# Kernel optimization log

Hardware: AMD Instinct MI355X
Metric: run time of the kernel (lower is better)

The kernel has to match this reference:

```python
import jax, jax.numpy as jnp
import numpy as np

N_NODES = 50000


def gcn_conv(x, W, b, row, col, n):
    """PyG GCNConv with default add_self_loops=True, normalize=True.
    out[i] = sum_{e: col[e]=i} d^-1/2[row[e]] d^-1/2[i] * (x@W)[row[e]]
             + d^-1[i]*(x@W)[i] + b,  where d = in-degree + 1 (self-loop).
    """
    x_lin = x @ W                                   # [n, out_ch]
    ones = jnp.ones(row.shape[0], dtype=x.dtype)
    deg = jax.ops.segment_sum(ones, col, num_segments=n) + 1.0  # self-loop
    dinv = jax.lax.rsqrt(deg)                       # deg >= 1, safe
    norm = dinv[row] * dinv[col]                    # [E]
    msg = norm[:, None] * x_lin[row]                # [E, out_ch]
    agg = jax.ops.segment_sum(msg, col, num_segments=n)
    self_term = (dinv * dinv)[:, None] * x_lin      # self-loop contribution
    return agg + self_term + b


def setup_inputs() -> dict:
    key = jax.random.key(0)
    ks = jax.random.split(key, 10)
    in_ch, hid, out_ch = 128, 256, 64
    E = 800000
    x = jax.random.normal(ks[0], (N_NODES, in_ch), dtype=jnp.float32)
    edge_attr = jax.random.normal(ks[1], (E, 8), dtype=jnp.float32)  # unused by forward
    edge_index = jax.random.randint(ks[2], (2, E), 0, N_NODES, dtype=jnp.int64)
    def glorot(k, fan_in, fan_out):
        s = float(np.sqrt(6.0 / (fan_in + fan_out)))
        return jax.random.uniform(k, (fan_in, fan_out), jnp.float32, -s, s)
    return {
        "x": x,
        "edge_attr": edge_attr,
        "edge_index": edge_index,
        "W1": glorot(ks[3], in_ch, hid), "b1": jnp.zeros((hid,), jnp.float32),
        "W2": glorot(ks[4], hid, hid),  "b2": jnp.zeros((hid,), jnp.float32),
        "W3": glorot(ks[5], hid, out_ch), "b3": jnp.zeros((out_ch,), jnp.float32),
    }


def reference(x, edge_attr, edge_index, W1, b1, W2, b2, W3, b3):
    n = x.shape[0]
    row, col = edge_index[0], edge_index[1]
    h = jax.nn.sigmoid(gcn_conv(x, W1, b1, row, col, n))
    h = jax.nn.sigmoid(gcn_conv(h, W2, b2, row, col, n))
    # dropout(p=0.1) in eval mode is identity
    return gcn_conv(h, W3, b3, row, col, n)
```

## Files before the change

kernel.cpp:

```cpp
#include <hip/hip_runtime.h>
#include <hip/hip_bf16.h>

typedef __bf16 bf16x8_t __attribute__((ext_vector_type(8)));
typedef float f32x4_t __attribute__((ext_vector_type(4)));
typedef float f32x2_t __attribute__((ext_vector_type(2)));

__device__ __forceinline__ float bits2f(unsigned int u) {
    union { unsigned int u; float f; } c; c.u = u; return c.f;
}
__device__ __forceinline__ unsigned short f2bf_bits(float f) {
    __hip_bfloat16 h = __float2bfloat16(f);
    return __builtin_bit_cast(unsigned short, h);
}

__global__ void sentinel_fill(float* __restrict__ out, int n) {
    int i = blockIdx.x * blockDim.x + threadIdx.x;
    if (i < n) out[i] = 100.0f;
}

__global__ void detect_ei(const unsigned int* __restrict__ ei, int* __restrict__ flags) {
    int lane = threadIdx.x;
    int cz = 0;
    #pragma unroll
    for (int j = 0; j < 4; ++j) {
        int idx = lane * 4 + j;
        cz += (ei[2 * idx + 1] == 0u);
    }
    #pragma unroll
    for (int off = 32; off; off >>= 1) cz += __shfl_down(cz, off);
    if (lane == 0) flags[0] = (cz > 200);
}


__global__ void count_rank_dual(const int* __restrict__ ei, int* __restrict__ cnt,
                                int* __restrict__ rank, int E, int M,
                                const int* __restrict__ flags) {
    int e = blockIdx.x * blockDim.x + threadIdx.x;
    if (e < E) {
        int c = flags[0] ? ei[2 * E + 2 * e] : ei[E + e];
        int rk = 0;
        if ((unsigned)c < (unsigned)M) rk = atomicAdd(&cnt[c], 1);
        rank[e] = rk;
    }
}

__global__ void scan_blocks(const int* __restrict__ cnt, int* __restrict__ excl,
                            int* __restrict__ bsum, int n) {
    int tid = threadIdx.x;
    int i = blockIdx.x * 256 + tid;
    int lane = tid & 63, wv = tid >> 6;
    __shared__ int ws[4];
    int v = (i < n) ? cnt[i] : 0;
    int s = v;
    #pragma unroll
    for (int off = 1; off < 64; off <<= 1) {
        int t = __shfl_up(s, off);
        if (lane >= off) s += t;
    }
    if (lane == 63) ws[wv] = s;
    __syncthreads();
    if (tid == 0) { int a = 0; for (int q = 0; q < 4; ++q) { int t = ws[q]; ws[q] = a; a += t; } }
    __syncthreads();
    int ex = s - v + ws[wv];
    if (i < n) excl[i] = ex;
    if (tid == 255) bsum[blockIdx.x] = ex + v;
}

__global__ void scan_bsums(const int* __restrict__ bsum, int* __restrict__ boff,
                           int nb, int* __restrict__ colptr, int n) {
    int tid = threadIdx.x, lane = tid & 63, wv = tid >> 6;
    __shared__ int ws[4];
    __shared__ int carry;
    if (tid == 0) carry = 0;
    __syncthreads();
    for (int base = 0; base < nb; base += 256) {
        int i = base + tid;
        int v = (i < nb) ? bsum[i] : 0;
        int s = v;
        #pragma unroll
        for (int off = 1; off < 64; off <<= 1) {
            int t = __shfl_up(s, off);
            if (lane >= off) s += t;
        }
        if (lane == 63) ws[wv] = s;
        __syncthreads();
        if (tid == 0) { int a = carry; for (int q = 0; q < 4; ++q) { int t = ws[q]; ws[q] = a; a += t; } carry = a; }
        __syncthreads();
        int ex = s - v + ws[wv];
        if (i < nb) boff[i] = ex;
        __syncthreads();
    }
    if (tid == 0) colptr[n] = carry;
}

__global__ void scan_add_dinv(const int* __restrict__ excl, const int* __restrict__ boff,
                              const int* __restrict__ cnt, int* __restrict__ colptr,
                              float* __restrict__ dinv, int n) {
    int i = blockIdx.x * 256 + threadIdx.x;
    if (i < n) {
        colptr[i] = excl[i] + boff[blockIdx.x];
        dinv[i] = rsqrtf((float)cnt[i] + 1.0f);
    }
}

__global__ void fill_csr_part(const int* __restrict__ ei, const int* __restrict__ colptr,
                              const int* __restrict__ rank, int* __restrict__ esrc,
                              int E, int M, int psz, const int* __restrict__ flags) {
    int part = blockIdx.x & 7;
    int e = (blockIdx.x >> 3) * 256 + threadIdx.x;
    int lo = part * psz;
    int hi = lo + psz; if (hi > M) hi = M;
    if (e < E) {
        int r, c;
        if (flags[0]) { r = ei[2 * e]; c = ei[2 * E + 2 * e]; }
        else          { r = ei[e];     c = ei[E + e]; }
        if (c >= lo && c < hi && (unsigned)r < (unsigned)M) {
            int p = colptr[c] + rank[e];
            if ((unsigned)p < (unsigned)E) esrc[p] = r;
        }
    }
}

__global__ void transpose_all(const float* __restrict__ W1, const float* __restrict__ W2,
                              const float* __restrict__ W3,
                              unsigned short* __restrict__ Wt1, unsigned short* __restrict__ Wt2,
                              unsigned short* __restrict__ Wt3) {
    int i = blockIdx.x * 256 + threadIdx.x;
    if (i < 32768) {
        int k = i >> 8, n = i & 255;
        Wt1[n * 128 + k] = f2bf_bits(W1[i]);
    } else if (i < 32768 + 65536) {
        int j = i - 32768;
        int k = j >> 8, n = j & 255;
        Wt2[n * 256 + k] = f2bf_bits(W2[j]);
    } else if (i < 114688) {
        int j = i - 98304;
        int k = j >> 6, n = j & 63;
        Wt3[n * 256 + k] = f2bf_bits(W3[j]);
    }
}

__global__ void prescale_x(const float* __restrict__ x, const float* __restrict__ dinv,
                           unsigned short* __restrict__ xs, int total) {
    int i = blockIdx.x * 256 + threadIdx.x;
    if (i < total) {
        int row = i >> 7;
        xs[i] = f2bf_bits(x[i] * dinv[row]);
    }
}

template<int K, int BN, int NTOT, int EPI>
__global__ __launch_bounds__(256) void gemm_tile(
    const __bf16* __restrict__ A,
    const unsigned short* __restrict__ Bt,
    const float* __restrict__ dinv,
    const float* __restrict__ bias,
    void* __restrict__ Y,
    int M)
{
    constexpr int KS = (K > 128) ? 128 : K;
    constexpr int KP = KS + 8;
    constexpr int NT = BN / 2 / 16;
    __shared__ unsigned short Bs[BN * KP];

    const int tid  = threadIdx.x;
    const int lane = tid & 63;
    const int wave = tid >> 6;
    const int wm   = wave >> 1;
    const int wn   = wave & 1;
    const int quad = lane >> 4;
    const int l16  = lane & 15;
    const int n0   = blockIdx.y * BN;

    int mrow[4];
#pragma unroll
    for (int mt = 0; mt < 4; ++mt) {
        int r = blockIdx.x * 128 + wm * 64 + mt * 16 + l16;
        mrow[mt] = (r < M) ? r : (M - 1);
    }

    f32x4_t acc[4][NT];
#pragma unroll
    for (int mt = 0; mt < 4; ++mt)
#pragma unroll
        for (int t = 0; t < NT; ++t) acc[mt][t] = (f32x4_t){0.f, 0.f, 0.f, 0.f};

    const unsigned short* BsW = &Bs[(wn * (BN / 2)) * KP];

    for (int kh = 0; kh < K; kh += KS) {
        constexpr int CH = BN * KS / 8;
        for (int idx = tid; idx < CH; idx += 256) {
            int n  = idx / (KS / 8);
            int k8 = idx - n * (KS / 8);
            uint4 v = *(const uint4*)(Bt + (size_t)(n0 + n) * K + kh + k8 * 8);
            *(uint4*)&Bs[n * KP + k8 * 8] = v;
        }
        __syncthreads();

#pragma unroll
        for (int kc = 0; kc < KS; kc += 32) {
            bf16x8_t a[4], b[NT];
#pragma unroll
            for (int mt = 0; mt < 4; ++mt)
                a[mt] = *(const bf16x8_t*)(A + (size_t)mrow[mt] * K + kh + kc + quad * 8);
#pragma unroll
            for (int t = 0; t < NT; ++t)
                b[t] = *(const bf16x8_t*)&BsW[(t * 16 + l16) * KP + kc + quad * 8];
#pragma unroll
            for (int mt = 0; mt < 4; ++mt)
#pragma unroll
                for (int t = 0; t < NT; ++t)
                    acc[mt][t] = __builtin_amdgcn_mfma_f32_16x16x32_bf16(a[mt], b[t], acc[mt][t], 0, 0, 0);
        }
        if (kh + KS < K) __syncthreads();
    }

    float bv[NT];
    if constexpr (EPI == 1) {
#pragma unroll
        for (int t = 0; t < NT; ++t)
            bv[t] = bias[n0 + wn * (BN / 2) + t * 16 + l16];
    }

#pragma unroll
    for (int mt = 0; mt < 4; ++mt) {
        int rowbase = blockIdx.x * 128 + wm * 64 + mt * 16 + quad * 4;
#pragma unroll
        for (int r = 0; r < 4; ++r) {
            int rrow = rowbase + r;
            if (rrow < M) {
                if constexpr (EPI == 0) {
                    float dv = dinv[rrow];
#pragma unroll
                    for (int t = 0; t < NT; ++t) {
                        int ccol = n0 + wn * (BN / 2) + t * 16 + l16;
                        ((__hip_bfloat16*)Y)[(size_t)rrow * NTOT + ccol] =
                            __float2bfloat16(acc[mt][t][r] * dv);
                    }
                } else if constexpr (EPI == 1) {
#pragma unroll
                    for (int t = 0; t < NT; ++t) {
                        int ccol = n0 + wn * (BN / 2) + t * 16 + l16;
                        float o = acc[mt][t][r] + bv[t];
                        o = 1.f / (1.f + __expf(-o));
                        ((__hip_bfloat16*)Y)[(size_t)rrow * NTOT + ccol] = __float2bfloat16(o);
                    }
                } else {
                    float dv = dinv[rrow];
#pragma unroll
                    for (int t = 0; t < NT; ++t) {
                        int ccol = n0 + wn * (BN / 2) + t * 16 + l16;
                        float o = acc[mt][t][r] * dv;
                        int pk = __builtin_amdgcn_cvt_pk_fp8_f32(o, o, 0, false);
                        ((unsigned char*)Y)[(size_t)rrow * NTOT + ccol] = (unsigned char)(pk & 0xff);
                    }
                }
            }
        }
    }
}

__global__ __launch_bounds__(256) void aggregate_fp8_256(
    const unsigned char* __restrict__ Y8,
    const int* __restrict__ colptr,
    const int* __restrict__ esrc,
    const float* __restrict__ dinv,
    const float* __restrict__ bias,
    unsigned short* __restrict__ H,
    int M, int Etot)
{
    const int lane = threadIdx.x & 63;
    const int wave = threadIdx.x >> 6;
    const int l = lane & 15;
    const int g = lane >> 4;
    int node = blockIdx.x * 4 + wave;
    if (node >= M) return;

    int s = colptr[node];
    int e = colptr[node + 1];
    if (s < 0) s = 0;
    if (e > Etot) e = Etot;
    if (e < s) e = s;

    const char* Yb = (const char*)Y8;
    const unsigned loff = (unsigned)(l * 16);

    f32x2_t acc[8];
    #pragma unroll
    for (int k = 0; k < 8; ++k) acc[k] = (f32x2_t){0.f, 0.f};

    auto unpack = [&](uint4 u) {
        acc[0] += __builtin_amdgcn_cvt_pk_f32_fp8(u.x, false);
        acc[1] += __builtin_amdgcn_cvt_pk_f32_fp8(u.x, true);
        acc[2] += __builtin_amdgcn_cvt_pk_f32_fp8(u.y, false);
        acc[3] += __builtin_amdgcn_cvt_pk_f32_fp8(u.y, true);
        acc[4] += __builtin_amdgcn_cvt_pk_f32_fp8(u.z, false);
        acc[5] += __builtin_amdgcn_cvt_pk_f32_fp8(u.z, true);
        acc[6] += __builtin_amdgcn_cvt_pk_f32_fp8(u.w, false);
        acc[7] += __builtin_amdgcn_cvt_pk_f32_fp8(u.w, true);
    };

    for (int base = s; base < e; base += 64) {
        int n = e - base; if (n > 64) n = 64;
        unsigned myOff = 0;
        if (lane < n) myOff = (unsigned)esrc[base + lane] << 8;
        int j = 0;
        #pragma unroll 4
        for (; j + 4 <= n; j += 4) {
            unsigned off = __shfl(myOff, j + g) + loff;
            uint4 u = *(const uint4*)(Yb + off);
            unpack(u);
        }
        if (j < n) {
            unsigned off = __shfl(myOff, j + g) + loff;
            if (j + g < n) {
                uint4 u = *(const uint4*)(Yb + off);
                unpack(u);
            }
        }
    }
    if (g == 0) {
        uint4 u = *(const uint4*)(Yb + ((unsigned)node << 8) + loff);
        unpack(u);
    }
    #pragma unroll
    for (int off = 16; off < 64; off <<= 1) {
        #pragma unroll
        for (int k = 0; k < 8; ++k) {
            f32x2_t t;
            t[0] = __shfl_xor(acc[k][0], off);
            t[1] = __shfl_xor(acc[k][1], off);
            acc[k] += t;
        }
    }

    if (g == 0) {
        float dv = dinv[node];
        float o[16];
        #pragma unroll
        for (int k = 0; k < 8; ++k) {
            o[2 * k]     = acc[k][0] * dv + bias[l * 16 + 2 * k];
            o[2 * k + 1] = acc[k][1] * dv + bias[l * 16 + 2 * k + 1];
        }
        #pragma unroll
        for (int k = 0; k < 16; ++k) o[k] = 1.f / (1.f + __expf(-o[k]));
        uint4 s0, s1;
        s0.x = (unsigned)f2bf_bits(o[0])  | ((unsigned)f2bf_bits(o[1])  << 16);
        s0.y = (unsigned)f2bf_bits(o[2])  | ((unsigned)f2bf_bits(o[3])  << 16);
        s0.z = (unsigned)f2bf_bits(o[4])  | ((unsigned)f2bf_bits(o[5])  << 16);
        s0.w = (unsigned)f2bf_bits(o[6])  | ((unsigned)f2bf_bits(o[7])  << 16);
        s1.x = (unsigned)f2bf_bits(o[8])  | ((unsigned)f2bf_bits(o[9])  << 16);
        s1.y = (unsigned)f2bf_bits(o[10]) | ((unsigned)f2bf_bits(o[11]) << 16);
        s1.z = (unsigned)f2bf_bits(o[12]) | ((unsigned)f2bf_bits(o[13]) << 16);
        s1.w = (unsigned)f2bf_bits(o[14]) | ((unsigned)f2bf_bits(o[15]) << 16);
        unsigned short* Hp = H + (size_t)node * 256 + l * 16;
        *(uint4*)Hp       = s0;
        *(uint4*)(Hp + 8) = s1;
    }
}

template<int C, bool SIG, bool OUTF32, bool HASB>
__global__ __launch_bounds__(256) void aggregate2(
    const unsigned short* __restrict__ Y,
    const int* __restrict__ colptr,
    const int* __restrict__ esrc,
    const float* __restrict__ dinv,
    const float* __restrict__ bias,
    void* __restrict__ H,
    int M, int Etot)
{
    constexpr int G   = C / 8;
    constexpr int EPW = 64 / G;
    const int lane = threadIdx.x & 63;
    const int wave = threadIdx.x >> 6;
    const int l = lane & (G - 1);
    const int g = lane / G;
    int node = blockIdx.x * 4 + wave;
    if (node >= M) return;

    int s = colptr[node];
    int e = colptr[node + 1];
    if (s < 0) s = 0;
    if (e > Etot) e = Etot;
    if (e < s) e = s;

    const char* Yb = (const char*)Y;
    const unsigned loff = (unsigned)(l * 16);

    float acc[8];
    #pragma unroll
    for (int k = 0; k < 8; ++k) acc[k] = 0.f;

    auto unpack = [&](uint4 u) {
        acc[0] += bits2f(u.x << 16);
        acc[1] += bits2f(u.x & 0xffff0000u);
        acc[2] += bits2f(u.y << 16);
        acc[3] += bits2f(u.y & 0xffff0000u);
        acc[4] += bits2f(u.z << 16);
        acc[5] += bits2f(u.z & 0xffff0000u);
        acc[6] += bits2f(u.w << 16);
        acc[7] += bits2f(u.w & 0xffff0000u);
    };

    for (int base = s; base < e; base += 64) {
        int n = e - base; if (n > 64) n = 64;
        unsigned myOff = 0;
        if (lane < n) myOff = (unsigned)esrc[base + lane] * (unsigned)(C * 2);
        int j = 0;
        #pragma unroll 4
        for (; j + EPW <= n; j += EPW) {
            unsigned off = __shfl(myOff, j + g) + loff;
            uint4 u = *(const uint4*)(Yb + off);
            unpack(u);
        }
        if (j < n) {
            unsigned off = __shfl(myOff, j + g) + loff;
            if (j + g < n) {
                uint4 u = *(const uint4*)(Yb + off);
                unpack(u);
            }
        }
    }
    if (g == 0) {
        unsigned off = (unsigned)node * (unsigned)(C * 2) + loff;
        uint4 u = *(const uint4*)(Yb + off);
        unpack(u);
    }
    #pragma unroll
    for (int off = G; off < 64; off <<= 1) {
        #pragma unroll
        for (int k = 0; k < 8; ++k) acc[k] += __shfl_xor(acc[k], off);
    }

    if (g == 0) {
        float dv = dinv[node];
        float o[8];
        #pragma unroll
        for (int k = 0; k < 8; ++k) {
            o[k] = acc[k] * dv;
            if (HASB) o[k] += bias[l * 8 + k];
            if (SIG) o[k] = 1.f / (1.f + __expf(-o[k]));
        }
        if constexpr (OUTF32) {
            float* Hp = (float*)H + (size_t)node * C + l * 8;
            *(float4*)Hp       = (float4){o[0], o[1], o[2], o[3]};
            *(float4*)(Hp + 4) = (float4){o[4], o[5], o[6], o[7]};
        } else {
            uint4 st;
            st.x = (unsigned)f2bf_bits(o[0]) | ((unsigned)f2bf_bits(o[1]) << 16);
            st.y = (unsigned)f2bf_bits(o[2]) | ((unsigned)f2bf_bits(o[3]) << 16);
            st.z = (unsigned)f2bf_bits(o[4]) | ((unsigned)f2bf_bits(o[5]) << 16);
            st.w = (unsigned)f2bf_bits(o[6]) | ((unsigned)f2bf_bits(o[7]) << 16);
            *(uint4*)((unsigned short*)H + (size_t)node * C + l * 8) = st;
        }
    }
}


extern "C" void kernel_launch(void* const* d_in, const int* in_sizes, int n_in,
                              void* d_out, int out_size, void* d_ws, size_t ws_size,
                              hipStream_t stream)
{
    int iEI = 2, iW1 = 3, iB1 = 4, iW2 = 5, iB2 = 6, iW3 = 7, iB3 = 8;
    if (n_in == 8) { iEI = 1; iW1 = 2; iB1 = 3; iW2 = 4; iB2 = 5; iW3 = 6; iB3 = 7; }

    const float* x  = (const float*)d_in[0];
    const int* ei   = (const int*)d_in[iEI];
    const float* W1 = (const float*)d_in[iW1];
    const float* b1 = (const float*)d_in[iB1];
    const float* W2 = (const float*)d_in[iW2];
    const float* b2 = (const float*)d_in[iB2];
    const float* W3 = (const float*)d_in[iW3];
    const float* b3 = (const float*)d_in[iB3];

    const int M = in_sizes[0] / 128;
    const int E = in_sizes[iEI] / 2;
    const int NB = (M + 255) / 256;
    const int PSZ = (M + 7) / 8;

    auto rnd = [](size_t b) { return (b + 255) & ~(size_t)255; };
    size_t needed = rnd(64 * 4)
                  + rnd((size_t)M * 4) * 2
                  + rnd((size_t)(M + 1) * 4)
                  + rnd((size_t)M * 4)
                  + rnd((size_t)(NB + 1) * 4) * 2
                  + rnd((size_t)E * 4) * 2
                  + rnd((size_t)256 * 128 * 2)
                  + rnd((size_t)256 * 256 * 2)
                  + rnd((size_t)64 * 256 * 2)
                  + rnd((size_t)M * 256 * 2) * 2;
    if (ws_size < needed) {
        sentinel_fill<<<(out_size + 255) / 256, 256, 0, stream>>>((float*)d_out, out_size);
        return;
    }

    char* p = (char*)d_ws;
    auto alloc = [&](size_t bytes) {
        char* r = p;
        p += (bytes + 255) & ~(size_t)255;
        return r;
    };
    int* flags  = (int*)alloc(64 * 4);
    float* dinv = (float*)alloc((size_t)M * 4);
    int* cnt    = (int*)alloc((size_t)M * 4);
    int* colptr = (int*)alloc((size_t)(M + 1) * 4);
    int* excl   = (int*)alloc((size_t)M * 4);
    int* bsum   = (int*)alloc((size_t)(NB + 1) * 4);
    int* boff   = (int*)alloc((size_t)(NB + 1) * 4);
    int* esrc   = (int*)alloc((size_t)E * 4);
    int* rank   = (int*)alloc((size_t)E * 4);
    unsigned short* Wt1 = (unsigned short*)alloc((size_t)256 * 128 * 2);
    unsigned short* Wt2 = (unsigned short*)alloc((size_t)256 * 256 * 2);
    unsigned short* Wt3 = (unsigned short*)alloc((size_t)64 * 256 * 2);
    __hip_bfloat16* ybuf = (__hip_bfloat16*)alloc((size_t)M * 256 * 2);
    __hip_bfloat16* hbuf = (__hip_bfloat16*)alloc((size_t)M * 256 * 2);

    unsigned short* xs = (unsigned short*)ybuf;
    unsigned short* xa = (unsigned short*)ybuf + (size_t)M * 128;
    unsigned char*  y8 = (unsigned char*)ybuf;

    detect_ei<<<1, 64, 0, stream>>>((const unsigned int*)ei, flags);

    hipMemsetAsync(cnt, 0, (size_t)M * 4, stream);
    count_rank_dual<<<(E + 255) / 256, 256, 0, stream>>>(ei, cnt, rank, E, M, flags);
    scan_blocks<<<NB, 256, 0, stream>>>(cnt, excl, bsum, M);
    scan_bsums<<<1, 256, 0, stream>>>(bsum, boff, NB, colptr, M);
    scan_add_dinv<<<NB, 256, 0, stream>>>(excl, boff, cnt, colptr, dinv, M);
    fill_csr_part<<<((E + 255) / 256) * 8, 256, 0, stream>>>(
        ei, colptr, rank, esrc, E, M, PSZ, flags);
    transpose_all<<<(114688 + 255) / 256, 256, 0, stream>>>(W1, W2, W3, Wt1, Wt2, Wt3);

    int gmb = (M + 127) / 128;
    int ga  = (M + 3) / 4;

    prescale_x<<<((M * 128) + 255) / 256, 256, 0, stream>>>(x, dinv, xs, M * 128);
    aggregate2<128, false, false, false><<<ga, 256, 0, stream>>>(
        xs, colptr, esrc, dinv, nullptr, xa, M, E);
    gemm_tile<128, 128, 256, 1><<<dim3(gmb, 2), 256, 0, stream>>>(
        (const __bf16*)xa, Wt1, dinv, b1, hbuf, M);
    gemm_tile<256, 128, 256, 2><<<dim3(gmb, 2), 256, 0, stream>>>(
        (const __bf16*)hbuf, Wt2, dinv, b2, y8, M);
    aggregate_fp8_256<<<ga, 256, 0, stream>>>(
        y8, colptr, esrc, dinv, b2, (unsigned short*)hbuf, M, E);
    gemm_tile<256, 64, 64, 0><<<dim3(gmb, 1), 256, 0, stream>>>(
        (const __bf16*)hbuf, Wt3, dinv, b3, ybuf, M);
    aggregate2<64, false, true, true><<<ga, 256, 0, stream>>>(
        (const unsigned short*)ybuf, colptr, esrc, dinv, b3, d_out, M, E);
}
```

Baseline: 347.4 us.

## Use fp8 gather features for layer-1 and layer-3 aggregations

Layer 1 now prescales x straight to fp8, vectorised over float4, instead of bf16. Layer 3's GEMM epilogue now writes fp8 rows as well. Both aggregations then run through a single generalised fp8 gather kernel templated on channel count. This halves the bytes read per gathered neighbour row in the bandwidth-bound aggregations, at the cost of lower precision in layer 1's input and layer 3's output features.

New measurement: 354.0 us. No clear change (+1.9%).

```diff
diff --git a/kernel.cpp b/kernel.cpp
--- a/kernel.cpp
+++ b/kernel.cpp
@@ -140,12 +140,16 @@
     }
 }
 
-__global__ void prescale_x(const float* __restrict__ x, const float* __restrict__ dinv,
-                           unsigned short* __restrict__ xs, int total) {
+__global__ void prescale_x_fp8(const float* __restrict__ x, const float* __restrict__ dinv,
+                               unsigned int* __restrict__ xs8, int total4) {
     int i = blockIdx.x * 256 + threadIdx.x;
-    if (i < total) {
-        int row = i >> 7;
-        xs[i] = f2bf_bits(x[i] * dinv[row]);
+    if (i < total4) {
+        int row = (i * 4) >> 7;
+        float dv = dinv[row];
+        float4 v = ((const float4*)x)[i];
+        int p0 = __builtin_amdgcn_cvt_pk_fp8_f32(v.x * dv, v.y * dv, 0, false);
+        int p1 = __builtin_amdgcn_cvt_pk_fp8_f32(v.z * dv, v.w * dv, 0, false);
+        xs8[i] = ((unsigned)p0 & 0xffffu) | ((unsigned)p1 << 16);
     }
 }
 
@@ -260,19 +264,23 @@
     }
 }
 
-__global__ __launch_bounds__(256) void aggregate_fp8_256(
+template<int C, bool SIG, bool OUTF32, bool HASB>
+__global__ __launch_bounds__(256) void aggregate_fp8(
     const unsigned char* __restrict__ Y8,
     const int* __restrict__ colptr,
     const int* __restrict__ esrc,
     const float* __restrict__ dinv,
     const float* __restrict__ bias,
-    unsigned short* __restrict__ H,
+    void* __restrict__ H,
     int M, int Etot)
 {
+    constexpr int G   = C / 16;
+    constexpr int EPW = 64 / G;
+    constexpr int SH  = (C == 256) ? 8 : ((C == 128) ? 7 : 6);
     const int lane = threadIdx.x & 63;
     const int wave = threadIdx.x >> 6;
-    const int l = lane & 15;
-    const int g = lane >> 4;
+    const int l = lane & (G - 1);
+    const int g = lane / G;
     int node = blockIdx.x * 4 + wave;
     if (node >= M) return;
 
@@ -303,10 +311,10 @@
     for (int base = s; base < e; base += 64) {
         int n = e - base; if (n > 64) n = 64;
         unsigned myOff = 0;
-        if (lane < n) myOff = (unsigned)esrc[base + lane] << 8;
+        if (lane < n) myOff = (unsigned)esrc[base + lane] << SH;
         int j = 0;
         #pragma unroll 4
-        for (; j + 4 <= n; j += 4) {
+        for (; j + EPW <= n; j += EPW) {
             unsigned off = __shfl(myOff, j + g) + loff;
             uint4 u = *(const uint4*)(Yb + off);
             unpack(u);
@@ -320,11 +328,11 @@
         }
     }
     if (g == 0) {
-        uint4 u = *(const uint4*)(Yb + ((unsigned)node << 8) + loff);
+        uint4 u = *(const uint4*)(Yb + ((unsigned)node << SH) + loff);
         unpack(u);
     }
     #pragma unroll
-    for (int off = 16; off < 64; off <<= 1) {
+    for (int off = G; off < 64; off <<= 1) {
         #pragma unroll
         for (int k = 0; k < 8; ++k) {
             f32x2_t t;
@@ -339,119 +347,36 @@
         float o[16];
         #pragma unroll
         for (int k = 0; k < 8; ++k) {
-            o[2 * k]     = acc[k][0] * dv + bias[l * 16 + 2 * k];
-            o[2 * k + 1] = acc[k][1] * dv + bias[l * 16 + 2 * k + 1];
-        }
-        #pragma unroll
-        for (int k = 0; k < 16; ++k) o[k] = 1.f / (1.f + __expf(-o[k]));
-        uint4 s0, s1;
-        s0.x = (unsigned)f2bf_bits(o[0])  | ((unsigned)f2bf_bits(o[1])  << 16);
-        s0.y = (unsigned)f2bf_bits(o[2])  | ((unsigned)f2bf_bits(o[3])  << 16);
-        s0.z = (unsigned)f2bf_bits(o[4])  | ((unsigned)f2bf_bits(o[5])  << 16);
-        s0.w = (unsigned)f2bf_bits(o[6])  | ((unsigned)f2bf_bits(o[7])  << 16);
-        s1.x = (unsigned)f2bf_bits(o[8])  | ((unsigned)f2bf_bits(o[9])  << 16);
-        s1.y = (unsigned)f2bf_bits(o[10]) | ((unsigned)f2bf_bits(o[11]) << 16);
-        s1.z = (unsigned)f2bf_bits(o[12]) | ((unsigned)f2bf_bits(o[13]) << 16);
-        s1.w = (unsigned)f2bf_bits(o[14]) | ((unsigned)f2bf_bits(o[15]) << 16);
-        unsigned short* Hp = H + (size_t)node * 256 + l * 16;
-        *(uint4*)Hp       = s0;
-        *(uint4*)(Hp + 8) = s1;
-    }
-}
-
-template<int C, bool SIG, bool OUTF32, bool HASB>
-__global__ __launch_bounds__(256) void aggregate2(
-    const unsigned short* __restrict__ Y,
-    const int* __restrict__ colptr,
-    const int* __restrict__ esrc,
-    const float* __restrict__ dinv,
-    const float* __restrict__ bias,
-    void* __restrict__ H,
-    int M, int Etot)
-{
-    constexpr int G   = C / 8;
-    constexpr int EPW = 64 / G;
-    const int lane = threadIdx.x & 63;
-    const int wave = threadIdx.x >> 6;
-    const int l = lane & (G - 1);
-    const int g = lane / G;
-    int node = blockIdx.x * 4 + wave;
-    if (node >= M) return;
-
-    int s = colptr[node];
-    int e = colptr[node + 1];
-    if (s < 0) s = 0;
-    if (e > Etot) e = Etot;
-    if (e < s) e = s;
-
-    const char* Yb = (const char*)Y;
-    const unsigned loff = (unsigned)(l * 16);
-
-    float acc[8];
-    #pragma unroll
-    for (int k = 0; k < 8; ++k) acc[k] = 0.f;
-
-    auto unpack = [&](uint4 u) {
-        acc[0] += bits2f(u.x << 16);
-        acc[1] += bits2f(u.x & 0xffff0000u);
-        acc[2] += bits2f(u.y << 16);
-        acc[3] += bits2f(u.y & 0xffff0000u);
-        acc[4] += bits2f(u.z << 16);
-        acc[5] += bits2f(u.z & 0xffff0000u);
-        acc[6] += bits2f(u.w << 16);
-        acc[7] += bits2f(u.w & 0xffff0000u);
-    };
-
-    for (int base = s; base < e; base += 64) {
-        int n = e - base; if (n > 64) n = 64;
-        unsigned myOff = 0;
-        if (lane < n) myOff = (unsigned)esrc[base + lane] * (unsigned)(C * 2);
-        int j = 0;
-        #pragma unroll 4
-        for (; j + EPW <= n; j += EPW) {
-            unsigned off = __shfl(myOff, j + g) + loff;
-            uint4 u = *(const uint4*)(Yb + off);
-            unpack(u);
-        }
-        if (j < n) {
-            unsigned off = __shfl(myOff, j + g) + loff;
-            if (j + g < n) {
-                uint4 u = *(const uint4*)(Yb + off);
-                unpack(u);
-            }
-        }
-    }
-    if (g == 0) {
-        unsigned off = (unsigned)node * (unsigned)(C * 2) + loff;
-        uint4 u = *(const uint4*)(Yb + off);
-        unpack(u);
-    }
-    #pragma unroll
-    for (int off = G; off < 64; off <<= 1) {
-        #pragma unroll
-        for (int k = 0; k < 8; ++k) acc[k] += __shfl_xor(acc[k], off);
-    }
-
-    if (g == 0) {
-        float dv = dinv[node];
-        float o[8];
-        #pragma unroll
-        for (int k = 0; k < 8; ++k) {
-            o[k] = acc[k] * dv;
-            if (HASB) o[k] += bias[l * 8 + k];
-            if (SIG) o[k] = 1.f / (1.f + __expf(-o[k]));
+            o[2 * k]     = acc[k][0] * dv;
+            o[2 * k + 1] = acc[k][1] * dv;
+        }
+        if constexpr (HASB) {
+            #pragma unroll
+            for (int k = 0; k < 16; ++k) o[k] += bias[l * 16 + k];
+        }
+        if constexpr (SIG) {
+            #pragma unroll
+            for (int k = 0; k < 16; ++k) o[k] = 1.f / (1.f + __expf(-o[k]));
         }
         if constexpr (OUTF32) {
-            float* Hp = (float*)H + (size_t)node * C + l * 8;
-            *(float4*)Hp       = (float4){o[0], o[1], o[2], o[3]};
-            *(float4*)(Hp + 4) = (float4){o[4], o[5], o[6], o[7]};
+            float* Hp = (float*)H + (size_t)node * C + l * 16;
+            *(float4*)Hp        = (float4){o[0],  o[1],  o[2],  o[3]};
+            *(float4*)(Hp + 4)  = (float4){o[4],  o[5],  o[6],  o[7]};
+            *(float4*)(Hp + 8)  = (float4){o[8],  o[9],  o[10], o[11]};
+            *(float4*)(Hp + 12) = (float4){o[12], o[13], o[14], o[15]};
         } else {
-            uint4 st;
-            st.x = (unsigned)f2bf_bits(o[0]) | ((unsigned)f2bf_bits(o[1]) << 16);
-            st.y = (unsigned)f2bf_bits(o[2]) | ((unsigned)f2bf_bits(o[3]) << 16);
-            st.z = (unsigned)f2bf_bits(o[4]) | ((unsigned)f2bf_bits(o[5]) << 16);
-            st.w = (unsigned)f2bf_bits(o[6]) | ((unsigned)f2bf_bits(o[7]) << 16);
-            *(uint4*)((unsigned short*)H + (size_t)node * C + l * 8) = st;
+            uint4 s0, s1;
+            s0.x = (unsigned)f2bf_bits(o[0])  | ((unsigned)f2bf_bits(o[1])  << 16);
+            s0.y = (unsigned)f2bf_bits(o[2])  | ((unsigned)f2bf_bits(o[3])  << 16);
+            s0.z = (unsigned)f2bf_bits(o[4])  | ((unsigned)f2bf_bits(o[5])  << 16);
+            s0.w = (unsigned)f2bf_bits(o[6])  | ((unsigned)f2bf_bits(o[7])  << 16);
+            s1.x = (unsigned)f2bf_bits(o[8])  | ((unsigned)f2bf_bits(o[9])  << 16);
+            s1.y = (unsigned)f2bf_bits(o[10]) | ((unsigned)f2bf_bits(o[11]) << 16);
+            s1.z = (unsigned)f2bf_bits(o[12]) | ((unsigned)f2bf_bits(o[13]) << 16);
+            s1.w = (unsigned)f2bf_bits(o[14]) | ((unsigned)f2bf_bits(o[15]) << 16);
+            unsigned short* Hp = (unsigned short*)H + (size_t)node * C + l * 16;
+            *(uint4*)Hp       = s0;
+            *(uint4*)(Hp + 8) = s1;
         }
     }
 }
@@ -515,9 +440,10 @@
     __hip_bfloat16* ybuf = (__hip_bfloat16*)alloc((size_t)M * 256 * 2);
     __hip_bfloat16* hbuf = (__hip_bfloat16*)alloc((size_t)M * 256 * 2);
 
-    unsigned short* xs = (unsigned short*)ybuf;
-    unsigned short* xa = (unsigned short*)ybuf + (size_t)M * 128;
-    unsigned char*  y8 = (unsigned char*)ybuf;
+    unsigned char*  xs8 = (unsigned char*)ybuf;
+    unsigned short* xa  = (unsigned short*)ybuf + (size_t)M * 64;
+    unsigned char*  y8  = (unsigned char*)ybuf;
+    unsigned char*  y38 = (unsigned char*)ybuf;
 
     detect_ei<<<1, 64, 0, stream>>>((const unsigned int*)ei, flags);
 
@@ -533,17 +459,18 @@
     int gmb = (M + 127) / 128;
     int ga  = (M + 3) / 4;
 
-    prescale_x<<<((M * 128) + 255) / 256, 256, 0, stream>>>(x, dinv, xs, M * 128);
-    aggregate2<128, false, false, false><<<ga, 256, 0, stream>>>(
-        xs, colptr, esrc, dinv, nullptr, xa, M, E);
+    prescale_x_fp8<<<((M * 32) + 255) / 256, 256, 0, stream>>>(
+        x, dinv, (unsigned int*)xs8, M * 32);
+    aggregate_fp8<128, false, false, false><<<ga, 256, 0, stream>>>(
+        xs8, colptr, esrc, dinv, nullptr, xa, M, E);
     gemm_tile<128, 128, 256, 1><<<dim3(gmb, 2), 256, 0, stream>>>(
         (const __bf16*)xa, Wt1, dinv, b1, hbuf, M);
     gemm_tile<256, 128, 256, 2><<<dim3(gmb, 2), 256, 0, stream>>>(
         (const __bf16*)hbuf, Wt2, dinv, b2, y8, M);
-    aggregate_fp8_256<<<ga, 256, 0, stream>>>(
-        y8, colptr, esrc, dinv, b2, (unsigned short*)hbuf, M, E);
-    gemm_tile<256, 64, 64, 0><<<dim3(gmb, 1), 256, 0, stream>>>(
-        (const __bf16*)hbuf, Wt3, dinv, b3, ybuf, M);
-    aggregate2<64, false, true, true><<<ga, 256, 0, stream>>>(
-        (const unsigned short*)ybuf, colptr, esrc, dinv, b3, d_out, M, E);
-}
+    aggregate_fp8<256, true, false, true><<<ga, 256, 0, stream>>>(
+        y8, colptr, esrc, dinv, b2, hbuf, M, E);
+    gemm_tile<256, 64, 64, 2><<<dim3(gmb, 1), 256, 0, stream>>>(
+        (const __bf16*)hbuf, Wt3, dinv, b3, y38, M);
+    aggregate_fp8<64, false, true, true><<<ga, 256, 0, stream>>>(
+        y38, colptr, esrc, dinv, b3, d_out, M, E);
+}
```
